# Kernel tuning notes

Hardware: AMD Instinct MI355X
Metric: run time of the kernel (lower is better)

The kernel has to match this reference:

```python
import jax, jax.numpy as jnp
import numpy as np

NUM_USERS = 100000  # n_users; embedding table has NUM_USERS+1 rows
NUM_ITEMS = 50000
D = 64
N_LAYERS = 3
N_TOTAL = NUM_USERS + 1 + NUM_ITEMS  # 150001
N_EDGES = 2_000_000
BATCH = 8192


def setup_inputs() -> dict:
    key = jax.random.key(0)
    ks = jax.random.split(key, 8)
    users = jax.random.randint(ks[0], (BATCH,), 0, NUM_USERS + 1, dtype=jnp.int32)
    items = jax.random.randint(ks[1], (BATCH,), 0, NUM_ITEMS, dtype=jnp.int32)
    labels = jax.random.uniform(ks[2], (BATCH,), dtype=jnp.float32)
    edge_row = jax.random.randint(ks[3], (N_EDGES,), 0, N_TOTAL, dtype=jnp.int32)
    edge_col = jax.random.randint(ks[4], (N_EDGES,), 0, N_TOTAL, dtype=jnp.int32)
    # mimic symmetric-normalized adjacency values ~ 1/sqrt(du*di)
    edge_val = jax.random.uniform(ks[5], (N_EDGES,), dtype=jnp.float32) / 32.0
    user_emb = jax.random.normal(ks[6], (NUM_USERS + 1, D), dtype=jnp.float32) * 0.1
    item_emb = jax.random.normal(ks[7], (NUM_ITEMS, D), dtype=jnp.float32) * 0.1
    return {"users": users, "items": items, "labels": labels,
            "edge_row": edge_row, "edge_col": edge_col, "edge_val": edge_val,
            "user_emb": user_emb, "item_emb": item_emb}


def _computer(user_emb, item_emb, edge_row, edge_col, edge_val):
    # LightGCN propagation: all_emb <- A @ all_emb, layer-wise mean pooling
    all_emb = jnp.concatenate([user_emb, item_emb], axis=0)  # [N, D]
    embs = [all_emb]
    for _ in range(N_LAYERS):
        msg = edge_val[:, None] * all_emb[edge_col]  # [E, D]
        all_emb = jax.ops.segment_sum(msg, edge_row, num_segments=N_TOTAL)
        embs.append(all_emb)
    light_out = jnp.mean(jnp.stack(embs, axis=1), axis=1)  # [N, D]
    return light_out[:NUM_USERS + 1], light_out[NUM_USERS + 1:]


def reference(users, items, labels, edge_row, edge_col, edge_val, user_emb, item_emb):
    all_users, all_items = _computer(user_emb, item_emb, edge_row, edge_col, edge_val)
    u = all_users[users]  # [B, D]
    v = all_items[items]  # [B, D]
    gamma = jnp.sum(u * v, axis=1)  # logits [B]
    y = labels.astype(gamma.dtype)
    # BCEWithLogitsLoss (mean): max(x,0) - x*y + log1p(exp(-|x|))
    loss = jnp.mean(jnp.maximum(gamma, 0) - gamma * y + jnp.log1p(jnp.exp(-jnp.abs(gamma))))
    return loss
```

## Files before the change

### kernel.cpp

```cpp
#include <hip/hip_runtime.h>
#include <hip/hip_fp16.h>

#define D 64
#define RB 512
#define RB_SHIFT 9
#define COL_BITS 18
#define COL_MASK 0x3FFFF
#define CHUNK 4096
#define FT 512
#define SPAN_CAP 12288

typedef float floatx2 __attribute__((ext_vector_type(2)));

__global__ void convhist_kernel(const float* __restrict__ user_emb,
                                const float* __restrict__ item_emb,
                                unsigned char* __restrict__ tbl,
                                int n_user_rows, int n_total,
                                const int* __restrict__ row,
                                int* __restrict__ hist, int n_edges, int nb,
                                int* __restrict__ cursor,
                                float* __restrict__ out) {
    __shared__ int h[RB];
    int blk = blockIdx.x;
    if (blk == 0) {
        if (threadIdx.x < 2) cursor[threadIdx.x] = 0;
        if (threadIdx.x == 0) out[0] = 0.0f;
    }
    for (int i = threadIdx.x; i < nb; i += FT) h[i] = 0;
    __syncthreads();
    int s = blk * CHUNK;
    int e = min(s + CHUNK, n_edges);
    for (int k = s + threadIdx.x; k < e; k += FT)
        atomicAdd(&h[row[k] >> RB_SHIFT], 1);
    __syncthreads();
    for (int i = threadIdx.x; i < nb; i += FT)
        hist[blk * nb + i] = h[i];
    size_t t = (size_t)blk * FT + threadIdx.x;
    size_t total4 = (size_t)n_total * (D / 4);
    size_t user4 = (size_t)n_user_rows * (D / 4);
    size_t stride = (size_t)gridDim.x * FT;
    for (size_t i = t; i < total4; i += stride) {
        float4 v = (i < user4) ? reinterpret_cast<const float4*>(user_emb)[i]
                               : reinterpret_cast<const float4*>(item_emb)[i - user4];
        int o = __builtin_amdgcn_cvt_pk_fp8_f32(v.x, v.y, 0, false);
        o = __builtin_amdgcn_cvt_pk_fp8_f32(v.z, v.w, o, true);
        reinterpret_cast<unsigned*>(tbl)[i] = (unsigned)o;
    }
}

__global__ void col_alloc_kernel(int* __restrict__ hist,
                                 int* __restrict__ cstart, int* __restrict__ cend,
                                 int* __restrict__ cursor, int nb, int nblk) {
    int w = (blockIdx.x * blockDim.x + threadIdx.x) >> 6;
    int lane = threadIdx.x & 63;
    if (w >= nb) return;
    int ssum = 0;
    for (int blk = lane; blk < nblk; blk += 64)
        ssum += hist[blk * nb + w];
    for (int off = 32; off > 0; off >>= 1)
        ssum += __shfl_down(ssum, off, 64);
    int base = 0;
    if (lane == 0) base = atomicAdd(cursor, ssum);
    base = __shfl(base, 0, 64);
    int run = base;
    int total = __shfl(ssum, 0, 64);
    if (lane == 0) { cstart[w] = base; cend[w] = base + total; }
    for (int b0 = 0; b0 < nblk; b0 += 64) {
        int blk = b0 + lane;
        int v = (blk < nblk) ? hist[blk * nb + w] : 0;
        int inc = v;
#pragma unroll
        for (int off = 1; off < 64; off <<= 1) {
            int t = __shfl_up(inc, off, 64);
            if (lane >= off) inc += t;
        }
        if (blk < nblk) hist[blk * nb + w] = run + (inc - v);
        run += __shfl(inc, 63, 64);
    }
}

__global__ void fill_exact_kernel(const int* __restrict__ row, const int* __restrict__ col,
                                  const float* __restrict__ val, const int* __restrict__ hist,
                                  int2* __restrict__ stage, int n_edges, int nb) {
    __shared__ int hloc[RB];
    __shared__ int lbase[RB];
    __shared__ int gbase[RB];
    __shared__ int wsum[FT / 64];
    __shared__ int2 sdata[CHUNK];
    __shared__ int  saddr[CHUNK];
    int blk = blockIdx.x;
    int tid = threadIdx.x;
    int lane = tid & 63, wid = tid >> 6;
    for (int i = tid; i < nb; i += FT) {
        hloc[i] = 0;
        gbase[i] = hist[blk * nb + i];
    }
    __syncthreads();
    int s = blk * CHUNK;
    int e = min(s + CHUNK, n_edges);
    int cnt = e - s;
    int2 data[8];
    int bkt[8], rnk[8];
    int nloc = 0;
#pragma unroll
    for (int j = 0; j < 8; ++j) {
        int k = s + j * FT + tid;
        if (k < e) {
            int r = row[k];
            int b = r >> RB_SHIFT;
            data[nloc] = make_int2(col[k] | ((r & (RB - 1)) << COL_BITS),
                                   __float_as_int(val[k]));
            bkt[nloc] = b;
            rnk[nloc] = atomicAdd(&hloc[b], 1);
            ++nloc;
        }
    }
    __syncthreads();
    int v = (tid < nb) ? hloc[tid] : 0;
    int inc = v;
#pragma unroll
    for (int off = 1; off < 64; off <<= 1) {
        int t = __shfl_up(inc, off, 64);
        if (lane >= off) inc += t;
    }
    if (lane == 63) wsum[wid] = inc;
    __syncthreads();
    if (wid == 0) {
        int wv = (lane < FT / 64) ? wsum[lane] : 0;
        int wi = wv;
#pragma unroll
        for (int off = 1; off < FT / 64; off <<= 1) {
            int t = __shfl_up(wi, off, 64);
            if (lane >= off) wi += t;
        }
        if (lane < FT / 64) wsum[lane] = wi - wv;
    }
    __syncthreads();
    if (tid < nb) lbase[tid] = (inc - v) + wsum[wid];
    __syncthreads();
    for (int j = 0; j < nloc; ++j) {
        int b = bkt[j];
        int pos = lbase[b] + rnk[j];
        sdata[pos] = data[j];
        saddr[pos] = gbase[b] + rnk[j];
    }
    __syncthreads();
    for (int j = tid; j < cnt; j += FT)
        stage[saddr[j]] = sdata[j];
}

__global__ void bucket_pad_kernel(const int* __restrict__ cstart,
                                  const int* __restrict__ cend,
                                  const int2* __restrict__ stage,
                                  int2* __restrict__ offs,
                                  unsigned* __restrict__ pairs,
                                  int* __restrict__ cursor, int n_total) {
    __shared__ int sc[RB];
    __shared__ int wsum[RB / 64];
    __shared__ int pbase_s, ptot_s;
    __shared__ unsigned lp[SPAN_CAP];
    int b = blockIdx.x;
    int tid = threadIdx.x;
    int lane = tid & 63, wid = tid >> 6;
    int s = cstart[b], e = cend[b];
    sc[tid] = 0;
    __syncthreads();
    int meta[16], wbits[16], rnk[16];
    int myn = 0;
#pragma unroll
    for (int j = 0; j < 16; ++j) {
        int k = s + j * RB + tid;
        if (k < e) {
            int2 p = stage[k];
            meta[myn] = p.x;
            wbits[myn] = p.y;
            rnk[myn] = atomicAdd(&sc[p.x >> COL_BITS], 1);
            ++myn;
        }
    }
    __syncthreads();
    int cnt = sc[tid];
    int pad = (cnt + 7) & ~7;
    int inc = pad;
#pragma unroll
    for (int off = 1; off < 64; off <<= 1) {
        int t = __shfl_up(inc, off, 64);
        if (lane >= off) inc += t;
    }
    if (lane == 63) wsum[wid] = inc;
    __syncthreads();
    if (wid == 0) {
        int wv = (lane < RB / 64) ? wsum[lane] : 0;
        int wi = wv;
#pragma unroll
        for (int off = 1; off < RB / 64; off <<= 1) {
            int t = __shfl_up(wi, off, 64);
            if (lane >= off) wi += t;
        }
        if (lane < RB / 64) wsum[lane] = wi - wv;
    }
    __syncthreads();
    int incl = inc + wsum[wid];
    if (tid == RB - 1) {
        pbase_s = atomicAdd(cursor, incl);
        ptot_s = incl;
    }
    __syncthreads();
    int startl = incl - pad;
    int r = b * RB + tid;
    if (r < n_total) offs[r] = make_int2(pbase_s + startl, pbase_s + startl + pad);
    sc[tid] = startl;
    int ptot = ptot_s;
    for (int j = tid; j < ptot; j += RB) lp[j] = 0u;
    __syncthreads();
#pragma unroll
    for (int j = 0; j < 16; ++j) {
        if (j < myn) {
            int rl = meta[j] >> COL_BITS;
            int pos = sc[rl] + rnk[j];
            float w = __int_as_float(wbits[j]);
            int pk = __builtin_amdgcn_cvt_pk_fp8_f32(w, 0.0f, 0, false);
            lp[pos] = (unsigned)(meta[j] & COL_MASK) | ((unsigned)(pk & 0xFF) << 24);
        }
    }
    __syncthreads();
    for (int j = tid; j < ptot; j += RB)
        pairs[pbase_s + j] = lp[j];
}

__device__ __forceinline__ void fma8(uint2 raw, float w, float a[8]) {
    floatx2 f0 = __builtin_amdgcn_cvt_pk_f32_fp8((int)raw.x, false);
    floatx2 f1 = __builtin_amdgcn_cvt_pk_f32_fp8((int)raw.x, true);
    floatx2 f2 = __builtin_amdgcn_cvt_pk_f32_fp8((int)raw.y, false);
    floatx2 f3 = __builtin_amdgcn_cvt_pk_f32_fp8((int)raw.y, true);
    a[0] += w * f0[0]; a[1] += w * f0[1];
    a[2] += w * f1[0]; a[3] += w * f1[1];
    a[4] += w * f2[0]; a[5] += w * f2[1];
    a[6] += w * f3[0]; a[7] += w * f3[1];
}

__device__ __forceinline__ void gather8(const unsigned* __restrict__ pairs, int k,
                                        const uint2* __restrict__ s2, int sub,
                                        float a[8]) {
    uint4 qa = *reinterpret_cast<const uint4*>(pairs + k);
    uint4 qb = *reinterpret_cast<const uint4*>(pairs + k + 4);
    uint2 r0 = s2[(size_t)(qa.x & COL_MASK) * 8 + sub];
    uint2 r1 = s2[(size_t)(qa.y & COL_MASK) * 8 + sub];
    uint2 r2 = s2[(size_t)(qa.z & COL_MASK) * 8 + sub];
    uint2 r3 = s2[(size_t)(qa.w & COL_MASK) * 8 + sub];
    uint2 r4 = s2[(size_t)(qb.x & COL_MASK) * 8 + sub];
    uint2 r5 = s2[(size_t)(qb.y & COL_MASK) * 8 + sub];
    uint2 r6 = s2[(size_t)(qb.z & COL_MASK) * 8 + sub];
    uint2 r7 = s2[(size_t)(qb.w & COL_MASK) * 8 + sub];
    fma8(r0, __builtin_amdgcn_cvt_f32_fp8((int)qa.x, 3), a);
    fma8(r1, __builtin_amdgcn_cvt_f32_fp8((int)qa.y, 3), a);
    fma8(r2, __builtin_amdgcn_cvt_f32_fp8((int)qa.z, 3), a);
    fma8(r3, __builtin_amdgcn_cvt_f32_fp8((int)qa.w, 3), a);
    fma8(r4, __builtin_amdgcn_cvt_f32_fp8((int)qb.x, 3), a);
    fma8(r5, __builtin_amdgcn_cvt_f32_fp8((int)qb.y, 3), a);
    fma8(r6, __builtin_amdgcn_cvt_f32_fp8((int)qb.z, 3), a);
    fma8(r7, __builtin_amdgcn_cvt_f32_fp8((int)qb.w, 3), a);
}

__global__ void spmm_gather_kernel(const int2* __restrict__ offs,
                                   const unsigned* __restrict__ pairs,
                                   const unsigned char* __restrict__ src,
                                   unsigned char* __restrict__ dst, int n_total) {
    int t = blockIdx.x * blockDim.x + threadIdx.x;
    int r = t >> 4;
    int half = (t >> 3) & 1;
    int sub = t & 7;
    if (r >= n_total) return;
    int2 oo = offs[r];
    const uint2* s2 = reinterpret_cast<const uint2*>(src);
    float a[8] = {0.f, 0.f, 0.f, 0.f, 0.f, 0.f, 0.f, 0.f};
    for (int k = oo.x + half * 8; k < oo.y; k += 16)
        gather8(pairs, k, s2, sub, a);
#pragma unroll
    for (int i = 0; i < 8; ++i)
        a[i] += __shfl_xor(a[i], 8, 64);
    if (half == 0) {
        int ox = __builtin_amdgcn_cvt_pk_fp8_f32(a[0], a[1], 0, false);
        ox = __builtin_amdgcn_cvt_pk_fp8_f32(a[2], a[3], ox, true);
        int oy = __builtin_amdgcn_cvt_pk_fp8_f32(a[4], a[5], 0, false);
        oy = __builtin_amdgcn_cvt_pk_fp8_f32(a[6], a[7], oy, true);
        uint2 o = make_uint2((unsigned)ox, (unsigned)oy);
        reinterpret_cast<uint2*>(dst)[(size_t)r * 8 + sub] = o;
    }
}

__global__ void batch_loss_kernel(const int* __restrict__ users,
                                  const int* __restrict__ items,
                                  const int2* __restrict__ offs,
                                  const unsigned* __restrict__ pairs,
                                  const float* __restrict__ user_emb,
                                  const float* __restrict__ item_emb,
                                  const unsigned char* __restrict__ buf0,
                                  const unsigned char* __restrict__ buf1,
                                  const float* __restrict__ labels,
                                  float* __restrict__ out,
                                  int batch, int n_user_rows) {
    int t = blockIdx.x * blockDim.x + threadIdx.x;
    int b = t >> 3;
    int sub = t & 7;
    const uint2* s2 = reinterpret_cast<const uint2*>(buf1);
    const uint2* s0 = reinterpret_cast<const uint2*>(buf0);
    float lb = 0.0f;
    if (b < batch) {
        float uf[8], vf[8];
        int u = users[b];
        int it = items[b];
        {
            float4 e0 = reinterpret_cast<const float4*>(user_emb + (size_t)u * D)[sub * 2];
            float4 e1 = reinterpret_cast<const float4*>(user_emb + (size_t)u * D)[sub * 2 + 1];
            uf[0] = e0.x; uf[1] = e0.y; uf[2] = e0.z; uf[3] = e0.w;
            uf[4] = e1.x; uf[5] = e1.y; uf[6] = e1.z; uf[7] = e1.w;
            float4 f0 = reinterpret_cast<const float4*>(item_emb + (size_t)it * D)[sub * 2];
            float4 f1 = reinterpret_cast<const float4*>(item_emb + (size_t)it * D)[sub * 2 + 1];
            vf[0] = f0.x; vf[1] = f0.y; vf[2] = f0.z; vf[3] = f0.w;
            vf[4] = f1.x; vf[5] = f1.y; vf[6] = f1.z; vf[7] = f1.w;
        }
        int urow = u;
        int vrow = n_user_rows + it;
        fma8(s0[(size_t)urow * 8 + sub], 1.0f, uf);
        fma8(s2[(size_t)urow * 8 + sub], 1.0f, uf);
        fma8(s0[(size_t)vrow * 8 + sub], 1.0f, vf);
        fma8(s2[(size_t)vrow * 8 + sub], 1.0f, vf);
        float au[8] = {0.f, 0.f, 0.f, 0.f, 0.f, 0.f, 0.f, 0.f};
        float av[8] = {0.f, 0.f, 0.f, 0.f, 0.f, 0.f, 0.f, 0.f};
        int2 ou = offs[urow];
        int2 ov = offs[vrow];
        for (int k = ou.x; k < ou.y; k += 8) gather8(pairs, k, s2, sub, au);
        for (int k = ov.x; k < ov.y; k += 8) gather8(pairs, k, s2, sub, av);
        float partial = 0.0f;
#pragma unroll
        for (int i = 0; i < 8; ++i)
            partial += (uf[i] + au[i]) * (vf[i] + av[i]);
        partial += __shfl_xor(partial, 1, 64);
        partial += __shfl_xor(partial, 2, 64);
        partial += __shfl_xor(partial, 4, 64);
        if (sub == 0) {
            float g = partial * (1.0f / 16.0f);
            float y = labels[b];
            lb = fmaxf(g, 0.0f) - g * y + log1pf(expf(-fabsf(g)));
        }
    }
    lb += __shfl_xor(lb, 8, 64);
    lb += __shfl_xor(lb, 16, 64);
    lb += __shfl_xor(lb, 32, 64);
    __shared__ float sd[4];
    int wid = threadIdx.x >> 6;
    if ((threadIdx.x & 63) == 0) sd[wid] = lb;
    __syncthreads();
    if (threadIdx.x == 0)
        atomicAdd(out, (sd[0] + sd[1] + sd[2] + sd[3]) / (float)batch);
}

extern "C" void kernel_launch(void* const* d_in, const int* in_sizes, int n_in,
                              void* d_out, int out_size, void* d_ws, size_t ws_size,
                              hipStream_t stream) {
    const int* users = (const int*)d_in[0];
    const int* items = (const int*)d_in[1];
    const float* labels = (const float*)d_in[2];
    const int* edge_row = (const int*)d_in[3];
    const int* edge_col = (const int*)d_in[4];
    const float* edge_val = (const float*)d_in[5];
    const float* user_emb = (const float*)d_in[6];
    const float* item_emb = (const float*)d_in[7];

    const int batch = in_sizes[0];
    const int n_edges = in_sizes[3];
    const int n_user_rows = in_sizes[6] / D;
    const int n_item_rows = in_sizes[7] / D;
    const int n_total = n_user_rows + n_item_rows;
    const int nb = (n_total + RB - 1) / RB;
    const int nblk = (n_edges + CHUNK - 1) / CHUNK;
    const int L = nb * nblk;
    const int max_pairs = n_edges + 7 * nb * RB;

    auto align256 = [](size_t x) { return (x + 255) & ~(size_t)255; };
    const size_t tblb_bytes = align256((size_t)n_total * D);
    const size_t offs_bytes = align256((size_t)n_total * sizeof(int2));
    const size_t pairs_bytes = align256((size_t)max_pairs * sizeof(unsigned));
    const size_t stage_bytes = align256((size_t)n_edges * sizeof(int2));
    const size_t hist_bytes = align256((size_t)L * sizeof(int));
    const size_t cse_bytes = align256((size_t)nb * sizeof(int));

    char* ws = (char*)d_ws;
    unsigned char* tbl  = (unsigned char*)ws;    ws += tblb_bytes;
    unsigned char* buf0 = (unsigned char*)ws;    ws += tblb_bytes;
    unsigned char* buf1 = (unsigned char*)ws;    ws += tblb_bytes;
    int2*  offs   = (int2*)ws;                   ws += offs_bytes;
    unsigned* pairs = (unsigned*)ws;             ws += pairs_bytes;
    int2*  stage  = (int2*)ws;                   ws += stage_bytes;
    int*   hist   = (int*)ws;                    ws += hist_bytes;
    int*   cstart = (int*)ws;                    ws += cse_bytes;
    int*   cend   = (int*)ws;                    ws += cse_bytes;
    int*   cursor = (int*)ws;                    ws += 256;

    convhist_kernel<<<nblk, FT, 0, stream>>>(user_emb, item_emb, tbl,
                                             n_user_rows, n_total,
                                             edge_row, hist, n_edges, nb,
                                             cursor, (float*)d_out);

    const int wave_blocks = (nb + 3) / 4;
    col_alloc_kernel<<<wave_blocks, 256, 0, stream>>>(hist, cstart, cend,
                                                      &cursor[0], nb, nblk);
    fill_exact_kernel<<<nblk, FT, 0, stream>>>(edge_row, edge_col, edge_val,
                                               hist, stage, n_edges, nb);
    bucket_pad_kernel<<<nb, RB, 0, stream>>>(cstart, cend, stage, offs, pairs,
                                             &cursor[1], n_total);

    const int spmm_blocks = (int)(((size_t)n_total * 16 + 255) / 256);
    spmm_gather_kernel<<<spmm_blocks, 256, 0, stream>>>(offs, pairs, tbl, buf0, n_total);
    spmm_gather_kernel<<<spmm_blocks, 256, 0, stream>>>(offs, pairs, buf0, buf1, n_total);

    const int bl_blocks = (batch * 8 + 255) / 256;
    batch_loss_kernel<<<bl_blocks, 256, 0, stream>>>(users, items, offs, pairs,
                                                     user_emb, item_emb, buf0, buf1,
                                                     labels, (float*)d_out,
                                                     batch, n_user_rows);
}
```

Baseline: 128.8 us.

## Shrink staging records to 6 bytes with early FP8 packing; interleave batch gathers

The fill kernel now converts edge weights to FP8 and packs them with the column index immediately. It writes a 4-byte packed word plus a 2-byte local-row array to staging, replacing the earlier 8-byte int2 records. This cuts global staging traffic between fill and bucket_pad and removes the conversion work from bucket_pad. The batch loss kernel also interleaves the user and item neighbor gathers to expose more memory-level parallelism. The split arrays add scattered 2-byte stores, which may coalesce less well than the single 8-byte stores.

```diff
diff --git a/kernel.cpp b/kernel.cpp
--- a/kernel.cpp
+++ b/kernel.cpp
@@ -81,13 +81,16 @@
 
 __global__ void fill_exact_kernel(const int* __restrict__ row, const int* __restrict__ col,
                                   const float* __restrict__ val, const int* __restrict__ hist,
-                                  int2* __restrict__ stage, int n_edges, int nb) {
+                                  unsigned* __restrict__ stageA,
+                                  unsigned short* __restrict__ stageB,
+                                  int n_edges, int nb) {
     __shared__ int hloc[RB];
     __shared__ int lbase[RB];
     __shared__ int gbase[RB];
     __shared__ int wsum[FT / 64];
-    __shared__ int2 sdata[CHUNK];
-    __shared__ int  saddr[CHUNK];
+    __shared__ unsigned sdA[CHUNK];
+    __shared__ unsigned short sdB[CHUNK];
+    __shared__ int saddr[CHUNK];
     int blk = blockIdx.x;
     int tid = threadIdx.x;
     int lane = tid & 63, wid = tid >> 6;
@@ -99,7 +102,8 @@
     int s = blk * CHUNK;
     int e = min(s + CHUNK, n_edges);
     int cnt = e - s;
-    int2 data[8];
+    unsigned dataA[8];
+    unsigned short dataB[8];
     int bkt[8], rnk[8];
     int nloc = 0;
 #pragma unroll
@@ -108,8 +112,9 @@
         if (k < e) {
             int r = row[k];
             int b = r >> RB_SHIFT;
-            data[nloc] = make_int2(col[k] | ((r & (RB - 1)) << COL_BITS),
-                                   __float_as_int(val[k]));
+            int pk = __builtin_amdgcn_cvt_pk_fp8_f32(val[k], 0.0f, 0, false);
+            dataA[nloc] = (unsigned)col[k] | ((unsigned)(pk & 0xFF) << 24);
+            dataB[nloc] = (unsigned short)(r & (RB - 1));
             bkt[nloc] = b;
             rnk[nloc] = atomicAdd(&hloc[b], 1);
             ++nloc;
@@ -141,17 +146,22 @@
     for (int j = 0; j < nloc; ++j) {
         int b = bkt[j];
         int pos = lbase[b] + rnk[j];
-        sdata[pos] = data[j];
+        sdA[pos] = dataA[j];
+        sdB[pos] = dataB[j];
         saddr[pos] = gbase[b] + rnk[j];
     }
     __syncthreads();
-    for (int j = tid; j < cnt; j += FT)
-        stage[saddr[j]] = sdata[j];
+    for (int j = tid; j < cnt; j += FT) {
+        int a = saddr[j];
+        stageA[a] = sdA[j];
+        stageB[a] = sdB[j];
+    }
 }
 
 __global__ void bucket_pad_kernel(const int* __restrict__ cstart,
                                   const int* __restrict__ cend,
-                                  const int2* __restrict__ stage,
+                                  const unsigned* __restrict__ stageA,
+                                  const unsigned short* __restrict__ stageB,
                                   int2* __restrict__ offs,
                                   unsigned* __restrict__ pairs,
                                   int* __restrict__ cursor, int n_total) {
@@ -165,16 +175,18 @@
     int s = cstart[b], e = cend[b];
     sc[tid] = 0;
     __syncthreads();
-    int meta[16], wbits[16], rnk[16];
+    unsigned metaA[16];
+    int rl[16], rnk[16];
     int myn = 0;
 #pragma unroll
     for (int j = 0; j < 16; ++j) {
         int k = s + j * RB + tid;
         if (k < e) {
-            int2 p = stage[k];
-            meta[myn] = p.x;
-            wbits[myn] = p.y;
-            rnk[myn] = atomicAdd(&sc[p.x >> COL_BITS], 1);
+            unsigned a = stageA[k];
+            int r = (int)stageB[k];
+            metaA[myn] = a;
+            rl[myn] = r;
+            rnk[myn] = atomicAdd(&sc[r], 1);
             ++myn;
         }
     }
@@ -215,13 +227,8 @@
     __syncthreads();
 #pragma unroll
     for (int j = 0; j < 16; ++j) {
-        if (j < myn) {
-            int rl = meta[j] >> COL_BITS;
-            int pos = sc[rl] + rnk[j];
-            float w = __int_as_float(wbits[j]);
-            int pk = __builtin_amdgcn_cvt_pk_fp8_f32(w, 0.0f, 0, false);
-            lp[pos] = (unsigned)(meta[j] & COL_MASK) | ((unsigned)(pk & 0xFF) << 24);
-        }
+        if (j < myn)
+            lp[sc[rl[j]] + rnk[j]] = metaA[j];
     }
     __syncthreads();
     for (int j = tid; j < ptot; j += RB)
@@ -330,8 +337,15 @@
         float av[8] = {0.f, 0.f, 0.f, 0.f, 0.f, 0.f, 0.f, 0.f};
         int2 ou = offs[urow];
         int2 ov = offs[vrow];
-        for (int k = ou.x; k < ou.y; k += 8) gather8(pairs, k, s2, sub, au);
-        for (int k = ov.x; k < ov.y; k += 8) gather8(pairs, k, s2, sub, av);
+        int ku = ou.x, kv = ov.x;
+        while (ku < ou.y && kv < ov.y) {
+            gather8(pairs, ku, s2, sub, au);
+            gather8(pairs, kv, s2, sub, av);
+            ku += 8;
+            kv += 8;
+        }
+        for (; ku < ou.y; ku += 8) gather8(pairs, ku, s2, sub, au);
+        for (; kv < ov.y; kv += 8) gather8(pairs, kv, s2, sub, av);
         float partial = 0.0f;
 #pragma unroll
         for (int i = 0; i < 8; ++i)
@@ -382,7 +396,8 @@
     const size_t tblb_bytes = align256((size_t)n_total * D);
     const size_t offs_bytes = align256((size_t)n_total * sizeof(int2));
     const size_t pairs_bytes = align256((size_t)max_pairs * sizeof(unsigned));
-    const size_t stage_bytes = align256((size_t)n_edges * sizeof(int2));
+    const size_t stA_bytes = align256((size_t)n_edges * sizeof(unsigned));
+    const size_t stB_bytes = align256((size_t)n_edges * sizeof(unsigned short));
     const size_t hist_bytes = align256((size_t)L * sizeof(int));
     const size_t cse_bytes = align256((size_t)nb * sizeof(int));
 
@@ -392,7 +407,8 @@
     unsigned char* buf1 = (unsigned char*)ws;    ws += tblb_bytes;
     int2*  offs   = (int2*)ws;                   ws += offs_bytes;
     unsigned* pairs = (unsigned*)ws;             ws += pairs_bytes;
-    int2*  stage  = (int2*)ws;                   ws += stage_bytes;
+    unsigned* stageA = (unsigned*)ws;            ws += stA_bytes;
+    unsigned short* stageB = (unsigned short*)ws; ws += stB_bytes;
     int*   hist   = (int*)ws;                    ws += hist_bytes;
     int*   cstart = (int*)ws;                    ws += cse_bytes;
     int*   cend   = (int*)ws;                    ws += cse_bytes;
@@ -407,9 +423,9 @@
     col_alloc_kernel<<<wave_blocks, 256, 0, stream>>>(hist, cstart, cend,
                                                       &cursor[0], nb, nblk);
     fill_exact_kernel<<<nblk, FT, 0, stream>>>(edge_row, edge_col, edge_val,
-                                               hist, stage, n_edges, nb);
-    bucket_pad_kernel<<<nb, RB, 0, stream>>>(cstart, cend, stage, offs, pairs,
-                                             &cursor[1], n_total);
+                                               hist, stageA, stageB, n_edges, nb);
+    bucket_pad_kernel<<<nb, RB, 0, stream>>>(cstart, cend, stageA, stageB,
+                                             offs, pairs, &cursor[1], n_total);
 
     const int spmm_blocks = (int)(((size_t)n_total * 16 + 255) / 256);
     spmm_gather_kernel<<<spmm_blocks, 256, 0, stream>>>(offs, pairs, tbl, buf0, n_total);
```

After: 131.2 us. About the same (+1.9%).
